# Kernel optimization log

Measured on AMD Instinct MI355X. Metric: run time of the kernel, lower is better.

Reference implementation:

```python
import jax, jax.numpy as jnp
import numpy as np

N = 50000
E = 1_600_000
HID = 128
NF = 128
NG = 64
CUTOFF = 10.0
LOG2 = float(np.log(2.0))
PI = float(np.pi)


def ssp(v):
    # ShiftedSoftplus: softplus(v) - log(2), numerically stable
    return jnp.logaddexp(v, 0.0) - LOG2


def setup_inputs() -> dict:
    key = jax.random.key(0)
    ks = jax.random.split(key, 12)
    s = 0.05
    x = jax.random.normal(ks[0], (N, HID), dtype=jnp.float32)
    edge_index = jax.random.randint(ks[1], (2, E), 0, N, dtype=jnp.int64 if jax.config.jax_enable_x64 else jnp.int32)
    edge_length = jax.random.uniform(ks[2], (E,), dtype=jnp.float32) * 12.0
    edge_attr = jax.random.normal(ks[3], (E, NG), dtype=jnp.float32)
    return {
        "x": x,
        "edge_index": edge_index,
        "edge_length": edge_length,
        "edge_attr": edge_attr,
        "lin1_w": jax.random.normal(ks[4], (HID, NF), dtype=jnp.float32) * s,
        "nn_w1": jax.random.normal(ks[5], (NG, NF), dtype=jnp.float32) * s,
        "nn_b1": jnp.zeros((NF,), dtype=jnp.float32),
        "nn_w2": jax.random.normal(ks[6], (NF, NF), dtype=jnp.float32) * s,
        "nn_b2": jnp.zeros((NF,), dtype=jnp.float32),
        "lin2_w": jax.random.normal(ks[7], (NF, HID), dtype=jnp.float32) * s,
        "lin2_b": jnp.zeros((HID,), dtype=jnp.float32),
        "lin_w": jax.random.normal(ks[8], (HID, HID), dtype=jnp.float32) * s,
        "lin_b": jnp.zeros((HID,), dtype=jnp.float32),
    }


def reference(x, edge_index, edge_length, edge_attr,
              lin1_w, nn_w1, nn_b1, nn_w2, nn_b2,
              lin2_w, lin2_b, lin_w, lin_b):
    # edge filter MLP: [E, NG] -> [E, NF]
    W = ssp(edge_attr @ nn_w1 + nn_b1) @ nn_w2 + nn_b2
    # cosine cutoff envelope
    C = 0.5 * (jnp.cos(edge_length * (PI / CUTOFF)) + 1.0)
    C = C * (edge_length <= CUTOFF) * (edge_length >= 0.0)
    W = W * C[:, None]
    # node projection, gather source, multiply, scatter-add to target
    h = x @ lin1_w                                   # [N, NF]
    src, dst = edge_index[0], edge_index[1]
    msg = h[src] * W                                 # [E, NF]
    agg = jax.ops.segment_sum(msg, dst, num_segments=N)  # [N, NF]
    out = agg @ lin2_w + lin2_b                      # [N, HID]
    out = ssp(out)
    out = out @ lin_w + lin_b
    return out
```

## Files before the change

kernel.cpp:

```cpp
#include <hip/hip_runtime.h>


typedef __attribute__((ext_vector_type(8))) short bf16x8;
typedef __attribute__((ext_vector_type(4))) float f32x4;

static __device__ __forceinline__ float sspf(float v) {
    return fmaxf(v, 0.0f) + __logf(1.0f + __expf(-fabsf(v))) - 0.69314718f;
}

static __device__ __forceinline__ short bf16s(float x) {
    unsigned u = __builtin_bit_cast(unsigned, x);
    return (short)((u + 0x7fffu + ((u >> 16) & 1u)) >> 16);
}

__global__ __launch_bounds__(256) void node_proj_kernel(
    const float* __restrict__ x, const float* __restrict__ w,
    float* __restrict__ h, int n)
{
    __shared__ float xsT[128 * 20];
    int row0 = blockIdx.x * 16;
    for (int i = threadIdx.x; i < 2048; i += 256) {
        int r = i >> 7, c = i & 127;
        int rr = row0 + r;
        xsT[c * 20 + r] = (rr < n) ? x[(size_t)rr * 128 + c] : 0.0f;
    }
    __syncthreads();
    int j = threadIdx.x & 127;
    int rb = (threadIdx.x >> 7) * 8;
    float acc[8] = {0, 0, 0, 0, 0, 0, 0, 0};
    for (int k = 0; k < 128; ++k) {
        float wk = w[k * 128 + j];
        const float4* xp = (const float4*)&xsT[k * 20 + rb];
        float4 u0 = xp[0], u1 = xp[1];
        acc[0] = fmaf(u0.x, wk, acc[0]);
        acc[1] = fmaf(u0.y, wk, acc[1]);
        acc[2] = fmaf(u0.z, wk, acc[2]);
        acc[3] = fmaf(u0.w, wk, acc[3]);
        acc[4] = fmaf(u1.x, wk, acc[4]);
        acc[5] = fmaf(u1.y, wk, acc[5]);
        acc[6] = fmaf(u1.z, wk, acc[6]);
        acc[7] = fmaf(u1.w, wk, acc[7]);
    }
#pragma unroll
    for (int r = 0; r < 8; ++r) {
        int rr = row0 + rb + r;
        if (rr < n) h[(size_t)rr * 128 + j] = acc[r];
    }
}

__global__ __launch_bounds__(512, 4) void edge_kernel(
    const float* __restrict__ eattr, const int* __restrict__ eidx,
    const float* __restrict__ elen,
    const float* __restrict__ w1, const float* __restrict__ b1,
    const float* __restrict__ w2, const float* __restrict__ b2,
    const float* __restrict__ h, float* __restrict__ agg, int E)
{
    __shared__ short w1T[128 * 72];
    __shared__ short w2T[128 * 136];
    __shared__ short tseg[8 * 16 * 40];

    for (int i = threadIdx.x; i < 64 * 128; i += 512) {
        int k = i >> 7, nn = i & 127;
        w1T[nn * 72 + k] = bf16s(w1[i]);
    }
    for (int i = threadIdx.x; i < 128 * 128; i += 512) {
        int k = i >> 7, nn = i & 127;
        w2T[nn * 136 + k] = bf16s(w2[i]);
    }
    __syncthreads();

    const int lane = threadIdx.x & 63;
    const int m = lane & 15;
    const int q = lane >> 4;
    short* tw = tseg + (threadIdx.x >> 6) * (16 * 40);

    float b1v[8], b2v[8];
#pragma unroll
    for (int u = 0; u < 8; ++u) {
        b1v[u] = b1[u * 16 + m];
        b2v[u] = b2[u * 16 + m];
    }

    const int ngroups = (E + 15) >> 4;
    int wid = blockIdx.x * 8 + (threadIdx.x >> 6);
    int stride = gridDim.x * 8;

    for (int g = wid; g < ngroups; g += stride) {
        int e0 = g << 4;

        int erow = e0 + m;
        if (erow >= E) erow = E - 1;
        const float* ap = eattr + (size_t)erow * 64 + q * 8;
        float4 x0 = *(const float4*)(ap);
        float4 x1 = *(const float4*)(ap + 4);
        float4 x2 = *(const float4*)(ap + 32);
        float4 x3 = *(const float4*)(ap + 36);
        bf16x8 af0, af1;
        af0[0] = bf16s(x0.x); af0[1] = bf16s(x0.y);
        af0[2] = bf16s(x0.z); af0[3] = bf16s(x0.w);
        af0[4] = bf16s(x1.x); af0[5] = bf16s(x1.y);
        af0[6] = bf16s(x1.z); af0[7] = bf16s(x1.w);
        af1[0] = bf16s(x2.x); af1[1] = bf16s(x2.y);
        af1[2] = bf16s(x2.z); af1[3] = bf16s(x2.w);
        af1[4] = bf16s(x3.x); af1[5] = bf16s(x3.y);
        af1[6] = bf16s(x3.z); af1[7] = bf16s(x3.w);

        float cvv[4];
        int sV[4], dV[4];
#pragma unroll
        for (int r = 0; r < 4; ++r) {
            int e = e0 + 4 * q + r;
            int ec = (e < E) ? e : 0;
            float len = elen[ec];
            sV[r] = eidx[ec];
            dV[r] = eidx[E + ec];
            bool ok = (e < E) && (len <= 10.0f) && (len >= 0.0f);
            cvv[r] = ok ? 0.5f * (__cosf(len * 0.31415927f) + 1.0f) : 0.0f;
        }

        f32x4 acc2[8];
#pragma unroll
        for (int nt = 0; nt < 8; ++nt) {
            f32x4 c; c[0] = b2v[nt]; c[1] = b2v[nt]; c[2] = b2v[nt]; c[3] = b2v[nt];
            acc2[nt] = c;
        }

#pragma unroll
        for (int k2 = 0; k2 < 4; ++k2) {
            f32x4 acc1[2];
#pragma unroll
            for (int t = 0; t < 2; ++t) {
                float bv = b1v[2 * k2 + t];
                f32x4 c; c[0] = bv; c[1] = bv; c[2] = bv; c[3] = bv;
                acc1[t] = c;
            }
#pragma unroll
            for (int t = 0; t < 2; ++t) {
#pragma unroll
                for (int a = 0; a < 2; ++a) {
                    bf16x8 bw = *(const bf16x8*)&w1T[(16 * (2 * k2 + t) + m) * 72 + a * 32 + q * 8];
                    acc1[t] = __builtin_amdgcn_mfma_f32_16x16x32_bf16(
                        (a == 0) ? af0 : af1, bw, acc1[t], 0, 0, 0);
                }
            }
#pragma unroll
            for (int t = 0; t < 2; ++t) {
#pragma unroll
                for (int r = 0; r < 4; ++r) {
                    tw[(4 * q + r) * 40 + 16 * t + m] = bf16s(sspf(acc1[t][r]));
                }
            }
            bf16x8 ta = *(const bf16x8*)&tw[m * 40 + q * 8];
#pragma unroll
            for (int nt = 0; nt < 8; ++nt) {
                bf16x8 bw2 = *(const bf16x8*)&w2T[(16 * nt + m) * 136 + k2 * 32 + q * 8];
                acc2[nt] = __builtin_amdgcn_mfma_f32_16x16x32_bf16(ta, bw2, acc2[nt], 0, 0, 0);
            }
        }

#pragma unroll
        for (int r = 0; r < 4; ++r) {
            float cv = cvv[r];
            if (cv != 0.0f) {
                const float* hp = h + (size_t)sV[r] * 128 + m;
                float* gp = agg + (size_t)dV[r] * 128 + m;
#pragma unroll
                for (int nt = 0; nt < 8; ++nt) {
                    float Wv = acc2[nt][r] * cv;
                    atomicAdd(gp + nt * 16, hp[nt * 16] * Wv);
                }
            }
        }
    }
}

__global__ __launch_bounds__(256) void out_kernel(
    const float* __restrict__ agg,
    const float* __restrict__ w2, const float* __restrict__ b2,
    const float* __restrict__ w3, const float* __restrict__ b3,
    float* __restrict__ out, int n)
{
    __shared__ float aT[128 * 20];
    __shared__ float mT[128 * 20];
    int row0 = blockIdx.x * 16;
    for (int i = threadIdx.x; i < 2048; i += 256) {
        int r = i >> 7, c = i & 127;
        int rr = row0 + r;
        aT[c * 20 + r] = (rr < n) ? agg[(size_t)rr * 128 + c] : 0.0f;
    }
    __syncthreads();
    int j = threadIdx.x & 127;
    int rb = (threadIdx.x >> 7) * 8;

    float acc[8];
    float bj = b2[j];
#pragma unroll
    for (int r = 0; r < 8; ++r) acc[r] = bj;
    for (int k = 0; k < 128; ++k) {
        float wk = w2[k * 128 + j];
        const float4* xp = (const float4*)&aT[k * 20 + rb];
        float4 u0 = xp[0], u1 = xp[1];
        acc[0] = fmaf(u0.x, wk, acc[0]);
        acc[1] = fmaf(u0.y, wk, acc[1]);
        acc[2] = fmaf(u0.z, wk, acc[2]);
        acc[3] = fmaf(u0.w, wk, acc[3]);
        acc[4] = fmaf(u1.x, wk, acc[4]);
        acc[5] = fmaf(u1.y, wk, acc[5]);
        acc[6] = fmaf(u1.z, wk, acc[6]);
        acc[7] = fmaf(u1.w, wk, acc[7]);
    }
    float4 s0, s1;
    s0.x = sspf(acc[0]); s0.y = sspf(acc[1]); s0.z = sspf(acc[2]); s0.w = sspf(acc[3]);
    s1.x = sspf(acc[4]); s1.y = sspf(acc[5]); s1.z = sspf(acc[6]); s1.w = sspf(acc[7]);
    ((float4*)&mT[j * 20 + rb])[0] = s0;
    ((float4*)&mT[j * 20 + rb])[1] = s1;
    __syncthreads();

    float bj3 = b3[j];
#pragma unroll
    for (int r = 0; r < 8; ++r) acc[r] = bj3;
    for (int k = 0; k < 128; ++k) {
        float wk = w3[k * 128 + j];
        const float4* xp = (const float4*)&mT[k * 20 + rb];
        float4 u0 = xp[0], u1 = xp[1];
        acc[0] = fmaf(u0.x, wk, acc[0]);
        acc[1] = fmaf(u0.y, wk, acc[1]);
        acc[2] = fmaf(u0.z, wk, acc[2]);
        acc[3] = fmaf(u0.w, wk, acc[3]);
        acc[4] = fmaf(u1.x, wk, acc[4]);
        acc[5] = fmaf(u1.y, wk, acc[5]);
        acc[6] = fmaf(u1.z, wk, acc[6]);
        acc[7] = fmaf(u1.w, wk, acc[7]);
    }
#pragma unroll
    for (int r = 0; r < 8; ++r) {
        int rr = row0 + rb + r;
        if (rr < n) out[(size_t)rr * 128 + j] = acc[r];
    }
}

extern "C" void kernel_launch(void* const* d_in, const int* in_sizes, int n_in,
                              void* d_out, int out_size, void* d_ws, size_t ws_size,
                              hipStream_t stream)
{
    const float* x     = (const float*)d_in[0];
    const int*   eidx  = (const int*)d_in[1];
    const float* elen  = (const float*)d_in[2];
    const float* eattr = (const float*)d_in[3];
    const float* lin1w = (const float*)d_in[4];
    const float* nnw1  = (const float*)d_in[5];
    const float* nnb1  = (const float*)d_in[6];
    const float* nnw2  = (const float*)d_in[7];
    const float* nnb2  = (const float*)d_in[8];
    const float* lin2w = (const float*)d_in[9];
    const float* lin2b = (const float*)d_in[10];
    const float* linw  = (const float*)d_in[11];
    const float* linb  = (const float*)d_in[12];

    int n = in_sizes[0] / 128;
    int E = in_sizes[2];

    float* h   = (float*)d_ws;
    float* agg = h + (size_t)n * 128;

    hipMemsetAsync(agg, 0, (size_t)n * 128 * sizeof(float), stream);

    node_proj_kernel<<<(n + 15) / 16, 256, 0, stream>>>(x, lin1w, h, n);
    edge_kernel<<<512, 512, 0, stream>>>(eattr, eidx, elen,
                                         nnw1, nnb1, nnw2, nnb2, h, agg, E);
    out_kernel<<<(n + 15) / 16, 256, 0, stream>>>(agg, lin2w, lin2b, linw, linb,
                                                  (float*)d_out, n);
}
```

Baseline: 1.244 ms.

## Replace atomic scatter with destination-sorted CSR pull aggregation

Builds a CSR by destination via histogram, scan and reorder kernels, then computes edge filters per destination node and accumulates messages in registers, writing each agg row once. This removes the per-edge float atomicAdds to agg and the agg memset. In exchange it adds three preprocessing kernels, a permuted gather of edge_attr, padding waste for partial 16-edge batches, and load imbalance from uneven node degrees.

Result: slower. 2.512 ms (+101.9%).

```diff
diff --git a/kernel.cpp b/kernel.cpp
--- a/kernel.cpp
+++ b/kernel.cpp
@@ -48,12 +48,81 @@
     }
 }
 
-__global__ __launch_bounds__(512, 4) void edge_kernel(
-    const float* __restrict__ eattr, const int* __restrict__ eidx,
-    const float* __restrict__ elen,
+__global__ __launch_bounds__(256) void hist_kernel(
+    const int* __restrict__ eidx, int* __restrict__ counts, int E)
+{
+    int i = blockIdx.x * 256 + threadIdx.x;
+    int stride = gridDim.x * 256;
+    for (; i < E; i += stride) atomicAdd(&counts[eidx[E + i]], 1);
+}
+
+__global__ __launch_bounds__(1024) void scan_kernel(
+    const int* __restrict__ counts, int* __restrict__ off,
+    int* __restrict__ cursor, int n)
+{
+    __shared__ int wsum[16];
+    __shared__ int carry_s;
+    int t = threadIdx.x;
+    int lane = t & 63, w = t >> 6;
+    if (t == 0) carry_s = 0;
+    __syncthreads();
+    for (int base = 0; base < n; base += 1024) {
+        int idx = base + t;
+        int v = (idx < n) ? counts[idx] : 0;
+        int s = v;
+#pragma unroll
+        for (int d = 1; d < 64; d <<= 1) {
+            int u = __shfl_up(s, d, 64);
+            if (lane >= d) s += u;
+        }
+        if (lane == 63) wsum[w] = s;
+        __syncthreads();
+        if (w == 0) {
+            int ws = (lane < 16) ? wsum[lane] : 0;
+#pragma unroll
+            for (int d = 1; d < 16; d <<= 1) {
+                int u = __shfl_up(ws, d, 64);
+                if (lane >= d) ws += u;
+            }
+            if (lane < 16) wsum[lane] = ws;
+        }
+        __syncthreads();
+        int waveoff = (w > 0) ? wsum[w - 1] : 0;
+        int total = wsum[15];
+        int excl = carry_s + waveoff + s - v;
+        if (idx < n) { off[idx] = excl; cursor[idx] = excl; }
+        __syncthreads();
+        if (t == 0) carry_s += total;
+        __syncthreads();
+    }
+    if (t == 0) off[n] = carry_s;
+}
+
+__global__ __launch_bounds__(256) void reorder_kernel(
+    const int* __restrict__ eidx, const float* __restrict__ elen,
+    int* __restrict__ cursor, int* __restrict__ srcS,
+    int* __restrict__ permS, float* __restrict__ cvS, int E)
+{
+    int i = blockIdx.x * 256 + threadIdx.x;
+    int stride = gridDim.x * 256;
+    for (; i < E; i += stride) {
+        int dst = eidx[E + i];
+        int pos = atomicAdd(&cursor[dst], 1);
+        srcS[pos] = eidx[i];
+        permS[pos] = i;
+        float len = elen[i];
+        bool ok = (len <= 10.0f) && (len >= 0.0f);
+        cvS[pos] = ok ? 0.5f * (__cosf(len * 0.31415927f) + 1.0f) : 0.0f;
+    }
+}
+
+__global__ __launch_bounds__(512, 4) void pull_kernel(
+    const float* __restrict__ eattr, const int* __restrict__ srcS,
+    const int* __restrict__ permS, const float* __restrict__ cvS,
+    const int* __restrict__ off,
     const float* __restrict__ w1, const float* __restrict__ b1,
     const float* __restrict__ w2, const float* __restrict__ b2,
-    const float* __restrict__ h, float* __restrict__ agg, int E)
+    const float* __restrict__ h, float* __restrict__ agg, int n)
 {
     __shared__ short w1T[128 * 72];
     __shared__ short w2T[128 * 136];
@@ -81,96 +150,113 @@
         b2v[u] = b2[u * 16 + m];
     }
 
-    const int ngroups = (E + 15) >> 4;
     int wid = blockIdx.x * 8 + (threadIdx.x >> 6);
-    int stride = gridDim.x * 8;
-
-    for (int g = wid; g < ngroups; g += stride) {
-        int e0 = g << 4;
-
-        int erow = e0 + m;
-        if (erow >= E) erow = E - 1;
-        const float* ap = eattr + (size_t)erow * 64 + q * 8;
-        float4 x0 = *(const float4*)(ap);
-        float4 x1 = *(const float4*)(ap + 4);
-        float4 x2 = *(const float4*)(ap + 32);
-        float4 x3 = *(const float4*)(ap + 36);
-        bf16x8 af0, af1;
-        af0[0] = bf16s(x0.x); af0[1] = bf16s(x0.y);
-        af0[2] = bf16s(x0.z); af0[3] = bf16s(x0.w);
-        af0[4] = bf16s(x1.x); af0[5] = bf16s(x1.y);
-        af0[6] = bf16s(x1.z); af0[7] = bf16s(x1.w);
-        af1[0] = bf16s(x2.x); af1[1] = bf16s(x2.y);
-        af1[2] = bf16s(x2.z); af1[3] = bf16s(x2.w);
-        af1[4] = bf16s(x3.x); af1[5] = bf16s(x3.y);
-        af1[6] = bf16s(x3.z); af1[7] = bf16s(x3.w);
-
-        float cvv[4];
-        int sV[4], dV[4];
-#pragma unroll
-        for (int r = 0; r < 4; ++r) {
-            int e = e0 + 4 * q + r;
-            int ec = (e < E) ? e : 0;
-            float len = elen[ec];
-            sV[r] = eidx[ec];
-            dV[r] = eidx[E + ec];
-            bool ok = (e < E) && (len <= 10.0f) && (len >= 0.0f);
-            cvv[r] = ok ? 0.5f * (__cosf(len * 0.31415927f) + 1.0f) : 0.0f;
+    int nwaves = gridDim.x * 8;
+
+    for (int node = wid; node < n; node += nwaves) {
+        int o0 = off[node], o1 = off[node + 1];
+        int d = o1 - o0;
+
+        float aggv[8] = {0, 0, 0, 0, 0, 0, 0, 0};
+
+        for (int b0 = 0; b0 < d; b0 += 16) {
+            int pa = o0 + b0 + m;
+            if (pa >= o1) pa = o1 - 1;
+            int pe = permS[pa];
+            const float* ap = eattr + (size_t)pe * 64 + q * 8;
+            float4 x0 = *(const float4*)(ap);
+            float4 x1 = *(const float4*)(ap + 4);
+            float4 x2 = *(const float4*)(ap + 32);
+            float4 x3 = *(const float4*)(ap + 36);
+            bf16x8 af0, af1;
+            af0[0] = bf16s(x0.x); af0[1] = bf16s(x0.y);
+            af0[2] = bf16s(x0.z); af0[3] = bf16s(x0.w);
+            af0[4] = bf16s(x1.x); af0[5] = bf16s(x1.y);
+            af0[6] = bf16s(x1.z); af0[7] = bf16s(x1.w);
+            af1[0] = bf16s(x2.x); af1[1] = bf16s(x2.y);
+            af1[2] = bf16s(x2.z); af1[3] = bf16s(x2.w);
+            af1[4] = bf16s(x3.x); af1[5] = bf16s(x3.y);
+            af1[6] = bf16s(x3.z); af1[7] = bf16s(x3.w);
+
+            float cvv[4];
+            int sV[4];
+#pragma unroll
+            for (int r = 0; r < 4; ++r) {
+                int p = o0 + b0 + 4 * q + r;
+                bool valid = (p < o1);
+                int pc = valid ? p : o1 - 1;
+                cvv[r] = valid ? cvS[pc] : 0.0f;
+                sV[r] = srcS[pc];
+            }
+
+            f32x4 acc2[8];
+#pragma unroll
+            for (int nt = 0; nt < 8; ++nt) {
+                f32x4 c; c[0] = b2v[nt]; c[1] = b2v[nt]; c[2] = b2v[nt]; c[3] = b2v[nt];
+                acc2[nt] = c;
+            }
+
+#pragma unroll
+            for (int k2 = 0; k2 < 4; ++k2) {
+                f32x4 acc1[2];
+#pragma unroll
+                for (int t = 0; t < 2; ++t) {
+                    float bv = b1v[2 * k2 + t];
+                    f32x4 c; c[0] = bv; c[1] = bv; c[2] = bv; c[3] = bv;
+                    acc1[t] = c;
+                }
+#pragma unroll
+                for (int t = 0; t < 2; ++t) {
+#pragma unroll
+                    for (int a = 0; a < 2; ++a) {
+                        bf16x8 bw = *(const bf16x8*)&w1T[(16 * (2 * k2 + t) + m) * 72 + a * 32 + q * 8];
+                        acc1[t] = __builtin_amdgcn_mfma_f32_16x16x32_bf16(
+                            (a == 0) ? af0 : af1, bw, acc1[t], 0, 0, 0);
+                    }
+                }
+#pragma unroll
+                for (int t = 0; t < 2; ++t) {
+#pragma unroll
+                    for (int r = 0; r < 4; ++r) {
+                        tw[(4 * q + r) * 40 + 16 * t + m] = bf16s(sspf(acc1[t][r]));
+                    }
+                }
+                bf16x8 ta = *(const bf16x8*)&tw[m * 40 + q * 8];
+#pragma unroll
+                for (int nt = 0; nt < 8; ++nt) {
+                    bf16x8 bw2 = *(const bf16x8*)&w2T[(16 * nt + m) * 136 + k2 * 32 + q * 8];
+                    acc2[nt] = __builtin_amdgcn_mfma_f32_16x16x32_bf16(ta, bw2, acc2[nt], 0, 0, 0);
+                }
+            }
+
+#pragma unroll
+            for (int r = 0; r < 4; ++r) {
+                float cv = cvv[r];
+                if (cv != 0.0f) {
+                    const float* hp = h + (size_t)sV[r] * 128 + m;
+#pragma unroll
+                    for (int nt = 0; nt < 8; ++nt) {
+                        aggv[nt] = fmaf(hp[nt * 16], acc2[nt][r] * cv, aggv[nt]);
+                    }
+                }
+            }
         }
 
-        f32x4 acc2[8];
 #pragma unroll
         for (int nt = 0; nt < 8; ++nt) {
-            f32x4 c; c[0] = b2v[nt]; c[1] = b2v[nt]; c[2] = b2v[nt]; c[3] = b2v[nt];
-            acc2[nt] = c;
+            float v = aggv[nt];
+            v += __shfl_xor(v, 16, 64);
+            v += __shfl_xor(v, 32, 64);
+            aggv[nt] = v;
         }
-
-#pragma unroll
-        for (int k2 = 0; k2 < 4; ++k2) {
-            f32x4 acc1[2];
-#pragma unroll
-            for (int t = 0; t < 2; ++t) {
-                float bv = b1v[2 * k2 + t];
-                f32x4 c; c[0] = bv; c[1] = bv; c[2] = bv; c[3] = bv;
-                acc1[t] = c;
-            }
-#pragma unroll
-            for (int t = 0; t < 2; ++t) {
-#pragma unroll
-                for (int a = 0; a < 2; ++a) {
-                    bf16x8 bw = *(const bf16x8*)&w1T[(16 * (2 * k2 + t) + m) * 72 + a * 32 + q * 8];
-                    acc1[t] = __builtin_amdgcn_mfma_f32_16x16x32_bf16(
-                        (a == 0) ? af0 : af1, bw, acc1[t], 0, 0, 0);
-                }
-            }
-#pragma unroll
-            for (int t = 0; t < 2; ++t) {
-#pragma unroll
-                for (int r = 0; r < 4; ++r) {
-                    tw[(4 * q + r) * 40 + 16 * t + m] = bf16s(sspf(acc1[t][r]));
-                }
-            }
-            bf16x8 ta = *(const bf16x8*)&tw[m * 40 + q * 8];
-#pragma unroll
-            for (int nt = 0; nt < 8; ++nt) {
-                bf16x8 bw2 = *(const bf16x8*)&w2T[(16 * nt + m) * 136 + k2 * 32 + q * 8];
-                acc2[nt] = __builtin_amdgcn_mfma_f32_16x16x32_bf16(ta, bw2, acc2[nt], 0, 0, 0);
-            }
-        }
-
-#pragma unroll
-        for (int r = 0; r < 4; ++r) {
-            float cv = cvv[r];
-            if (cv != 0.0f) {
-                const float* hp = h + (size_t)sV[r] * 128 + m;
-                float* gp = agg + (size_t)dV[r] * 128 + m;
-#pragma unroll
-                for (int nt = 0; nt < 8; ++nt) {
-                    float Wv = acc2[nt][r] * cv;
-                    atomicAdd(gp + nt * 16, hp[nt * 16] * Wv);
-                }
-            }
-        }
+        float wA, wB;
+        if (q == 0)      { wA = aggv[0]; wB = aggv[1]; }
+        else if (q == 1) { wA = aggv[2]; wB = aggv[3]; }
+        else if (q == 2) { wA = aggv[4]; wB = aggv[5]; }
+        else             { wA = aggv[6]; wB = aggv[7]; }
+        float* gp = agg + (size_t)node * 128;
+        gp[32 * q + m] = wA;
+        gp[32 * q + 16 + m] = wB;
     }
 }
 
@@ -260,14 +346,23 @@
     int n = in_sizes[0] / 128;
     int E = in_sizes[2];
 
-    float* h   = (float*)d_ws;
-    float* agg = h + (size_t)n * 128;
-
-    hipMemsetAsync(agg, 0, (size_t)n * 128 * sizeof(float), stream);
+    float* h      = (float*)d_ws;
+    float* agg    = h + (size_t)n * 128;
+    int*   counts = (int*)(agg + (size_t)n * 128);
+    int*   off    = counts + n;
+    int*   cursor = off + n + 1;
+    int*   srcS   = cursor + n;
+    int*   permS  = srcS + E;
+    float* cvS    = (float*)(permS + E);
+
+    hipMemsetAsync(counts, 0, (size_t)n * sizeof(int), stream);
 
     node_proj_kernel<<<(n + 15) / 16, 256, 0, stream>>>(x, lin1w, h, n);
-    edge_kernel<<<512, 512, 0, stream>>>(eattr, eidx, elen,
-                                         nnw1, nnb1, nnw2, nnb2, h, agg, E);
+    hist_kernel<<<2048, 256, 0, stream>>>(eidx, counts, E);
+    scan_kernel<<<1, 1024, 0, stream>>>(counts, off, cursor, n);
+    reorder_kernel<<<2048, 256, 0, stream>>>(eidx, elen, cursor, srcS, permS, cvS, E);
+    pull_kernel<<<512, 512, 0, stream>>>(eattr, srcS, permS, cvS, off,
+                                         nnw1, nnb1, nnw2, nnb2, h, agg, n);
     out_kernel<<<(n + 15) / 16, 256, 0, stream>>>(agg, lin2w, lin2b, linw, linb,
                                                   (float*)d_out, n);
 }
```
